# Kernel optimization log

Hardware: AMD Instinct MI355X
Metric: run time of the kernel (lower is better)

The kernel has to match this reference:

```python
import jax, jax.numpy as jnp
import numpy as np


def _rank_transform_ascending(flat):
    # torch: _, idx = sort(flat, descending=False); flat[idx] = linspace(0,1,n)+1/n
    n = flat.shape[0]
    order = jnp.argsort(flat)  # ascending
    prob = jnp.linspace(0.0, 1.0, n, dtype=flat.dtype) + jnp.asarray(1.0 / n, flat.dtype)
    return jnp.zeros_like(flat).at[order].set(prob)


def corr_attention(query, key, value):
    # score[b,h,i,j] = cosine-like similarity q_i . k_j / (|q_i| |k_j|)
    score = jnp.einsum('bhid,bhjd->bhij', query, key)
    q_len = jnp.sqrt(jnp.sum(query * query, axis=-1, keepdims=True)) + 1e-5  # [b,h,s,1]
    k_len = jnp.sqrt(jnp.sum(key * key, axis=-1, keepdims=True)) + 1e-5      # [b,h,s,1]
    score = score / (q_len * jnp.swapaxes(k_len, -1, -2))
    signal = jnp.sign(score)
    size = score.shape
    flat = jnp.abs(score).reshape(-1)
    ranked = _rank_transform_ascending(flat)
    score = -jnp.log(ranked).reshape(size) * signal
    score = score / jnp.sum(jnp.abs(score), axis=-1, keepdims=True)
    return jnp.einsum('bhij,bhjd->bhid', score, value)


def setup_inputs() -> dict:
    key0 = jax.random.key(0)
    kq, kk, kv = jax.random.split(key0, 3)
    B, H, S, D = 4, 8, 1024, 64
    query = jax.random.normal(kq, (B, H, S, D), dtype=jnp.float32)
    key = jax.random.normal(kk, (B, H, S, D), dtype=jnp.float32)
    value = jax.random.normal(kv, (B, H, S, D), dtype=jnp.float32)
    return {"query": query, "key": key, "value": value}


def reference(query, key, value):
    # Attention.forward with mode='season'
    return corr_attention(query, key, value)
```

## Files before the change

### kernel.cpp

```cpp
#include <hip/hip_runtime.h>
#include <math.h>
#include <stdint.h>

#define S_LEN 1024
#define D_DIM 64
#define BH    32
#define KSHIFT 13
#define NBINS 130048u
#define CODE_BASE 97280u
#define NB2   32768u
#define HIST_LO_C 20480u
#define NHOT_H  12288u
#define PV_LO_C 22528u
#define NPVT   10240u
#define NCHUNK 64
#define HBLK   256
#define INV_NM1 (1.0f/33554431.0f)
#define INV_N   (2.9802322387695312e-08f)
#define FIX_TH  1e-4f


typedef _Float16 half8 __attribute__((ext_vector_type(8)));
typedef short    short8 __attribute__((ext_vector_type(8)));
typedef float    floatx4 __attribute__((ext_vector_type(4)));

__device__ __forceinline__ void bf16_split(float x, short& hi, short& lo) {
  unsigned u = __float_as_uint(x);
  unsigned h = (u + 0x7FFFu + ((u >> 16) & 1u)) >> 16;
  float hf = __uint_as_float(h << 16);
  float lf = x - hf;
  hi = (short)h;
  lo = (short)(__float_as_uint(lf) >> 16);
}

__global__ __launch_bounds__(256) void norms_kernel(
    const float* __restrict__ Q, const float* __restrict__ K,
    double* __restrict__ qinvD, double* __restrict__ kinvD,
    unsigned short* __restrict__ Qhi_g, unsigned short* __restrict__ Qlo_g,
    unsigned short* __restrict__ Khi_g, unsigned short* __restrict__ Klo_g) {
  int row  = blockIdx.x * 4 + (threadIdx.x >> 6);
  int lane = threadIdx.x & 63;
  const float* src; double* dstD; unsigned short *hD, *lD; int r = row;
  if (row < BH * S_LEN) { src = Q; dstD = qinvD; hD = Qhi_g; lD = Qlo_g; }
  else { src = K; dstD = kinvD; hD = Khi_g; lD = Klo_g; r = row - BH * S_LEN; }
  float xf = src[(size_t)r * D_DIM + lane];
  double v = (double)xf;
  double s = v * v;
  #pragma unroll
  for (int off = 32; off; off >>= 1) s += __shfl_down(s, off);
  double inv = 0.0;
  if (lane == 0) {
    inv = 1.0 / (sqrt(s) + 1e-5);
    dstD[r] = inv;
  }
  inv = __shfl(inv, 0);
  float x = xf * (float)inv;
  short hi, lo;
  bf16_split(x, hi, lo);
  hD[(size_t)r * D_DIM + lane] = (unsigned short)hi;
  lD[(size_t)r * D_DIM + lane] = (unsigned short)lo;
}

__global__ __launch_bounds__(256) void qk_mfma_kernel(
    const float* __restrict__ Q, const float* __restrict__ K,
    const unsigned short* __restrict__ Qhi_g, const unsigned short* __restrict__ Qlo_g,
    const unsigned short* __restrict__ Khi_g, const unsigned short* __restrict__ Klo_g,
    const double* __restrict__ qinvD, const double* __restrict__ kinvD,
    unsigned short* __restrict__ code16) {
  __shared__ short Qhi[64][72], Qlo[64][72];
  __shared__ short Khi[64][72], Klo[64][72];
  int bh = blockIdx.z;
  int i0 = blockIdx.y * 64;
  int j0 = blockIdx.x * 64;
  int tid = threadIdx.x;
  {
    const unsigned short* Qh = Qhi_g + ((size_t)bh * S_LEN + i0) * D_DIM;
    const unsigned short* Ql = Qlo_g + ((size_t)bh * S_LEN + i0) * D_DIM;
    const unsigned short* Kh = Khi_g + ((size_t)bh * S_LEN + j0) * D_DIM;
    const unsigned short* Kl = Klo_g + ((size_t)bh * S_LEN + j0) * D_DIM;
    #pragma unroll
    for (int l = 0; l < 2; ++l) {
      int idx = l * 256 + tid;
      int row = idx >> 3, c = (idx & 7) * 8;
      *(uint4*)&Qhi[row][c] = *(const uint4*)(Qh + (size_t)row * D_DIM + c);
      *(uint4*)&Qlo[row][c] = *(const uint4*)(Ql + (size_t)row * D_DIM + c);
      *(uint4*)&Khi[row][c] = *(const uint4*)(Kh + (size_t)row * D_DIM + c);
      *(uint4*)&Klo[row][c] = *(const uint4*)(Kl + (size_t)row * D_DIM + c);
    }
  }
  __syncthreads();
  int wave = tid >> 6;
  int lane = tid & 63;
  int m    = lane & 15;
  int quad = lane >> 4;
  floatx4 acc[4];
  #pragma unroll
  for (int n = 0; n < 4; ++n) acc[n] = (floatx4){0.f, 0.f, 0.f, 0.f};
  #pragma unroll
  for (int ks = 0; ks < 2; ++ks) {
    int kb = ks * 32 + quad * 8;
    short8 a_hi = *(const short8*)&Qhi[wave * 16 + m][kb];
    short8 a_lo = *(const short8*)&Qlo[wave * 16 + m][kb];
    #pragma unroll
    for (int nt = 0; nt < 4; ++nt) {
      short8 b_hi = *(const short8*)&Khi[nt * 16 + m][kb];
      short8 b_lo = *(const short8*)&Klo[nt * 16 + m][kb];
      acc[nt] = __builtin_amdgcn_mfma_f32_16x16x32_bf16(a_hi, b_hi, acc[nt], 0, 0, 0);
      acc[nt] = __builtin_amdgcn_mfma_f32_16x16x32_bf16(a_hi, b_lo, acc[nt], 0, 0, 0);
      acc[nt] = __builtin_amdgcn_mfma_f32_16x16x32_bf16(a_lo, b_hi, acc[nt], 0, 0, 0);
    }
  }
  #pragma unroll
  for (int nt = 0; nt < 4; ++nt) {
    #pragma unroll
    for (int r = 0; r < 4; ++r) {
      unsigned long long am = __ballot(fabsf(acc[nt][r]) < FIX_TH);
      while (am) {
        int src = (int)(__ffsll((long long)am) - 1);
        am &= am - 1;
        int i_s = i0 + wave * 16 + (src >> 4) * 4 + r;
        int j_s = j0 + nt * 16 + (src & 15);
        double qd = (double)Q[((size_t)bh * S_LEN + i_s) * D_DIM + lane];
        double kd = (double)K[((size_t)bh * S_LEN + j_s) * D_DIM + lane];
        double pd = qd * kd;
        #pragma unroll
        for (int off = 32; off; off >>= 1) pd += __shfl_down(pd, off);
        float corr = 0.f;
        if (lane == 0)
          corr = (float)(pd * qinvD[(size_t)bh * S_LEN + i_s] * kinvD[(size_t)bh * S_LEN + j_s]);
        corr = __shfl(corr, 0);
        if (lane == src) acc[nt][r] = corr;
      }
    }
  }
  #pragma unroll
  for (int r = 0; r < 4; ++r) {
    unsigned short* op = code16 + (size_t)bh * 1048576 + (size_t)(j0 >> 6) * 65536
                       + (size_t)(i0 + wave * 16 + quad * 4 + r) * 64 + m;
    #pragma unroll
    for (int nt = 0; nt < 4; ++nt) {
      unsigned u = __float_as_uint(acc[nt][r]);
      unsigned a = u & 0x7fffffffu;
      unsigned b = a >> KSHIFT;
      if (b > NBINS - 1u) b = NBINS - 1u;
      unsigned c = (b < CODE_BASE) ? 0u : (b - CODE_BASE);
      op[nt * 16] = (unsigned short)(c | ((u >> 16) & 0x8000u));
    }
  }
}

__global__ __launch_bounds__(1024) void hist_kernel(
    const uint4* __restrict__ codes, unsigned* __restrict__ hist,
    unsigned char* __restrict__ partial) {
  __shared__ unsigned lh[NHOT_H];
  int tid = threadIdx.x;
  for (unsigned i = tid; i < NHOT_H; i += 1024) lh[i] = 0u;
  __syncthreads();
  const uint4* p = codes + (size_t)blockIdx.x * 16384;
  #pragma unroll 2
  for (int it = 0; it < 16; ++it) {
    uint4 w = p[it * 1024 + tid];
    unsigned ws[4] = {w.x, w.y, w.z, w.w};
    #pragma unroll
    for (int k = 0; k < 4; ++k) {
      unsigned c0 = ws[k] & 0x7fffu;
      unsigned c1 = (ws[k] >> 16) & 0x7fffu;
      if (c0 >= HIST_LO_C) atomicAdd(&lh[c0 - HIST_LO_C], 1u);
      else                 atomicAdd(&hist[c0], 1u);
      if (c1 >= HIST_LO_C) atomicAdd(&lh[c1 - HIST_LO_C], 1u);
      else                 atomicAdd(&hist[c1], 1u);
    }
  }
  __syncthreads();
  unsigned char* dst = partial + (size_t)blockIdx.x * NHOT_H;
  for (unsigned i = tid; i < NHOT_H; i += 1024) dst[i] = (unsigned char)lh[i];
}

__global__ __launch_bounds__(256) void hreduce_kernel(
    const unsigned char* __restrict__ partial, unsigned* __restrict__ hist) {
  unsigned bin = blockIdx.x * 256 + threadIdx.x;
  unsigned s = 0;
  #pragma unroll 8
  for (int b = 0; b < HBLK; ++b) s += (unsigned)partial[(size_t)b * NHOT_H + bin];
  hist[HIST_LO_C + bin] = s;
}

__global__ __launch_bounds__(256) void vt_kernel(
    const float* __restrict__ V, _Float16* __restrict__ Vt) {
  __shared__ _Float16 T[64][72];
  int bh = blockIdx.y, j0 = blockIdx.x * 64, tid = threadIdx.x;
  const float* Vb = V + ((size_t)bh * S_LEN + j0) * D_DIM;
  #pragma unroll
  for (int l = 0; l < 4; ++l) {
    int idx = l * 256 + tid;
    int jr = idx >> 4, d4 = idx & 15;
    float4 v = ((const float4*)Vb)[idx];
    T[d4*4+0][jr] = (_Float16)v.x;
    T[d4*4+1][jr] = (_Float16)v.y;
    T[d4*4+2][jr] = (_Float16)v.z;
    T[d4*4+3][jr] = (_Float16)v.w;
  }
  __syncthreads();
  _Float16* Ob = Vt + (size_t)(bh * 16 + blockIdx.x) * 4096;
  #pragma unroll
  for (int l = 0; l < 2; ++l) {
    int idx = l * 256 + tid;
    int d = idx >> 3, jc = idx & 7;
    uint4 val = *(const uint4*)&T[d][jc*8];
    *(uint4*)(Ob + (size_t)d * 64 + jc*8) = val;
  }
}

__global__ __launch_bounds__(256) void scan1_kernel(const unsigned* __restrict__ hist,
                                                    unsigned* __restrict__ csum) {
  __shared__ unsigned sd[256];
  int c = blockIdx.x, t = threadIdx.x;
  const unsigned* p = hist + (size_t)c * 512;
  sd[t] = p[t] + p[t + 256];
  __syncthreads();
  for (int off = 128; off; off >>= 1) {
    if (t < off) sd[t] += sd[t + off];
    __syncthreads();
  }
  if (t == 0) csum[c] = sd[0];
}

__global__ __launch_bounds__(256) void scan2_kernel(unsigned* __restrict__ csum) {
  __shared__ unsigned d[256];
  int t = threadIdx.x;
  unsigned v = (t < NCHUNK) ? csum[t] : 0u;
  d[t] = v; __syncthreads();
  for (int off = 1; off < 256; off <<= 1) {
    unsigned x = (t >= off) ? d[t - off] : 0u;
    __syncthreads();
    d[t] += x;
    __syncthreads();
  }
  if (t < NCHUNK) csum[t] = d[t] - v;
}

__global__ __launch_bounds__(256) void scan3_kernel(const unsigned* __restrict__ hist,
                                                    const unsigned* __restrict__ csum,
                                                    _Float16* __restrict__ tab2) {
  __shared__ unsigned ts[256];
  int c = blockIdx.x, t = threadIdx.x;
  const unsigned* p = hist + (size_t)c * 512 + t * 2;
  unsigned l0 = p[0], l1 = p[1];
  unsigned s = l0 + l1;
  ts[t] = s; __syncthreads();
  for (int off = 1; off < 256; off <<= 1) {
    unsigned x = (t >= off) ? ts[t - off] : 0u;
    __syncthreads();
    ts[t] += x;
    __syncthreads();
  }
  unsigned base = csum[c] + ts[t] - s;
  int idx = c * 512 + t * 2;
  float r0 = (float)base + 0.5f * ((float)l0 - 1.0f);
  tab2[idx]     = (_Float16)(-__logf(fmaf(r0, INV_NM1, INV_N)));
  float r1 = (float)(base + l0) + 0.5f * ((float)l1 - 1.0f);
  tab2[idx + 1] = (_Float16)(-__logf(fmaf(r1, INV_NM1, INV_N)));
}

__global__ __launch_bounds__(256) void pv_mfma_kernel(
    const unsigned short* __restrict__ code16, const _Float16* __restrict__ Vt,
    const unsigned short* __restrict__ tab2, float* __restrict__ out) {
  __shared__ unsigned short ldsT[NPVT];
  __shared__ float red[4352];
  int tid = threadIdx.x;

  int bh   = blockIdx.y;
  int wave = tid >> 6;
  int lane = tid & 63;
  int m    = lane & 15;
  int quad = lane >> 4;
  int i0   = blockIdx.x * 16;
  const unsigned short* Sb = code16 + (size_t)bh * 1048576 + (size_t)(i0 + m) * 64;
  const _Float16*       Vb = Vt + (size_t)bh * 65536;

  uint4 cw[8];
  #pragma unroll
  for (int ks = 0; ks < 8; ++ks) {
    int k0  = wave * 256 + ks * 32 + quad * 8;
    int jt  = k0 >> 6;
    int jin = k0 & 63;
    cw[ks] = *(const uint4*)(Sb + (size_t)jt * 65536 + jin);
  }

  {
    const unsigned* gsrc = (const unsigned*)(tab2 + PV_LO_C);
    unsigned* ldst = (unsigned*)ldsT;
    #pragma unroll
    for (int i = 0; i < 20; ++i)
      ldst[i * 256 + tid] = gsrc[i * 256 + tid];
  }
  __syncthreads();

  floatx4 acc[4];
  #pragma unroll
  for (int n = 0; n < 4; ++n) acc[n] = (floatx4){0.f, 0.f, 0.f, 0.f};
  float rsum = 0.f;

  #pragma unroll
  for (int ks = 0; ks < 8; ++ks) {
    int k0  = wave * 256 + ks * 32 + quad * 8;
    int jt  = k0 >> 6;
    int jin = k0 & 63;
    unsigned ww[4] = {cw[ks].x, cw[ks].y, cw[ks].z, cw[ks].w};
    union { unsigned short u[8]; half8 h; } af;
    #pragma unroll
    for (int e = 0; e < 8; ++e) {
      unsigned cd = (e & 1) ? (ww[e >> 1] >> 16) : (ww[e >> 1] & 0xffffu);
      unsigned c  = cd & 0x7fffu;
      unsigned sg = cd & 0x8000u;
      unsigned short tb;
      if (c >= PV_LO_C) tb = ldsT[c - PV_LO_C];
      else              tb = tab2[c];
      af.u[e] = (unsigned short)(tb ^ sg);
      unsigned short tabs = (unsigned short)(tb & 0x7fffu);
      _Float16 th = __builtin_bit_cast(_Float16, tabs);
      rsum += (float)th;
    }
    half8 bf[4];
    #pragma unroll
    for (int n = 0; n < 4; ++n)
      bf[n] = *(const half8*)(Vb + (size_t)jt * 4096 + (size_t)(n * 16 + m) * 64 + jin);
    #pragma unroll
    for (int n = 0; n < 4; ++n)
      acc[n] = __builtin_amdgcn_mfma_f32_16x16x32_f16(af.h, bf[n], acc[n], 0, 0, 0);
  }

  #pragma unroll
  for (int n = 0; n < 4; ++n)
    #pragma unroll
    for (int r = 0; r < 4; ++r)
      red[(wave * 16 + quad * 4 + r) * 64 + n * 16 + m] = acc[n][r];
  red[4096 + wave * 64 + lane] = rsum;
  __syncthreads();

  int col = tid & 63;
  int rq  = tid >> 6;
  #pragma unroll
  for (int t = 0; t < 4; ++t) {
    int row = rq * 4 + t;
    float s = 0.f;
    #pragma unroll
    for (int w = 0; w < 4; ++w) s += red[(w * 16 + row) * 64 + col];
    float rs = 0.f;
    #pragma unroll
    for (int w = 0; w < 4; ++w)
      #pragma unroll
      for (int q = 0; q < 4; ++q)
        rs += red[4096 + w * 64 + q * 16 + row];
    out[((size_t)bh * S_LEN + i0 + row) * D_DIM + col] = s / rs;
  }
}

extern "C" void kernel_launch(void* const* d_in, const int* in_sizes, int n_in,
                              void* d_out, int out_size, void* d_ws, size_t ws_size,
                              hipStream_t stream) {
  const float* Q = (const float*)d_in[0];
  const float* K = (const float*)d_in[1];
  const float* V = (const float*)d_in[2];
  float* out = (float*)d_out;
  char* ws = (char*)d_ws;
  unsigned short* code16  = (unsigned short*)(ws);
  unsigned*       hist    = (unsigned*)(ws + 67108864);
  unsigned char*  partial = (unsigned char*)(ws + 67239936);
  double*         qinvD   = (double*)(ws + 67239936 + 3145728);
  double*         kinvD   = (double*)(ws + 67239936 + 3407872);
  _Float16*       Vt      = (_Float16*)(ws + 67239936);
  unsigned*       csum    = (unsigned*)(ws + 67239936 + 4194304);
  _Float16*       tab2    = (_Float16*)(ws + 67239936 + 4195328);
  unsigned short* Qhi_g   = (unsigned short*)(ws + 71503872);
  unsigned short* Qlo_g   = (unsigned short*)(ws + 75698176);
  unsigned short* Khi_g   = (unsigned short*)(ws + 79892480);
  unsigned short* Klo_g   = (unsigned short*)(ws + 84086784);

  hipMemsetAsync(hist, 0, NB2 * sizeof(unsigned), stream);
  norms_kernel<<<(2 * BH * S_LEN) / 4, 256, 0, stream>>>(
      Q, K, qinvD, kinvD, Qhi_g, Qlo_g, Khi_g, Klo_g);
  qk_mfma_kernel<<<dim3(16, 16, BH), 256, 0, stream>>>(
      Q, K, Qhi_g, Qlo_g, Khi_g, Klo_g, qinvD, kinvD, code16);
  hist_kernel<<<HBLK, 1024, 0, stream>>>((const uint4*)code16, hist, partial);
  hreduce_kernel<<<NHOT_H / 256, 256, 0, stream>>>(partial, hist);
  vt_kernel<<<dim3(16, BH), 256, 0, stream>>>(V, Vt);
  scan1_kernel<<<NCHUNK, 256, 0, stream>>>(hist, csum);
  scan2_kernel<<<1, 256, 0, stream>>>(csum);
  scan3_kernel<<<NCHUNK, 256, 0, stream>>>(hist, csum, tab2);
  pv_mfma_kernel<<<dim3(S_LEN / 16, BH), 256, 0, stream>>>(
      code16, Vt, (const unsigned short*)tab2, out);
}
```

Before: 198.3 us.

## Stage code tiles in LDS and prefetch all V fragments before compute

The PV kernel now loads its 16-row code tile with fully coalesced 16-byte loads and stages it in shared memory. The table slice is loaded with vectorized uint4 loads. All V fragments for the eight k-steps are issued up front, so global latency overlaps before the MFMA loop. This raises register pressure (32 half8 values held live) and LDS usage by 32 KB, and launch bounds now request 2 blocks per CU, which may limit occupancy or cause spills.

```diff
diff --git a/kernel.cpp b/kernel.cpp
--- a/kernel.cpp
+++ b/kernel.cpp
@@ -262,10 +262,11 @@
   tab2[idx + 1] = (_Float16)(-__logf(fmaf(r1, INV_NM1, INV_N)));
 }
 
-__global__ __launch_bounds__(256) void pv_mfma_kernel(
+__global__ __launch_bounds__(256, 2) void pv_mfma_kernel(
     const unsigned short* __restrict__ code16, const _Float16* __restrict__ Vt,
     const unsigned short* __restrict__ tab2, float* __restrict__ out) {
   __shared__ unsigned short ldsT[NPVT];
+  __shared__ unsigned short codeT[16384];
   __shared__ float red[4352];
   int tid = threadIdx.x;
 
@@ -275,25 +276,38 @@
   int m    = lane & 15;
   int quad = lane >> 4;
   int i0   = blockIdx.x * 16;
-  const unsigned short* Sb = code16 + (size_t)bh * 1048576 + (size_t)(i0 + m) * 64;
+  const unsigned short* Cb = code16 + (size_t)bh * 1048576;
   const _Float16*       Vb = Vt + (size_t)bh * 65536;
 
-  uint4 cw[8];
+  uint4 ctmp[8];
+  #pragma unroll
+  for (int p = 0; p < 8; ++p) {
+    int c = p * 256 + tid;
+    int jt = c >> 7, row = (c >> 3) & 15, cin = c & 7;
+    ctmp[p] = *(const uint4*)(Cb + (size_t)jt * 65536 + (size_t)(i0 + row) * 64 + cin * 8);
+  }
+  uint4 ttmp[5];
+  #pragma unroll
+  for (int p = 0; p < 5; ++p)
+    ttmp[p] = *(const uint4*)(tab2 + PV_LO_C + (size_t)(p * 256 + tid) * 8);
+
+  half8 bf[8][4];
   #pragma unroll
   for (int ks = 0; ks < 8; ++ks) {
     int k0  = wave * 256 + ks * 32 + quad * 8;
     int jt  = k0 >> 6;
     int jin = k0 & 63;
-    cw[ks] = *(const uint4*)(Sb + (size_t)jt * 65536 + jin);
-  }
-
-  {
-    const unsigned* gsrc = (const unsigned*)(tab2 + PV_LO_C);
-    unsigned* ldst = (unsigned*)ldsT;
-    #pragma unroll
-    for (int i = 0; i < 20; ++i)
-      ldst[i * 256 + tid] = gsrc[i * 256 + tid];
-  }
+    #pragma unroll
+    for (int n = 0; n < 4; ++n)
+      bf[ks][n] = *(const half8*)(Vb + (size_t)jt * 4096 + (size_t)(n * 16 + m) * 64 + jin);
+  }
+
+  #pragma unroll
+  for (int p = 0; p < 8; ++p)
+    *(uint4*)&codeT[(p * 256 + tid) * 8] = ctmp[p];
+  #pragma unroll
+  for (int p = 0; p < 5; ++p)
+    *(uint4*)&ldsT[(p * 256 + tid) * 8] = ttmp[p];
   __syncthreads();
 
   floatx4 acc[4];
@@ -306,7 +320,8 @@
     int k0  = wave * 256 + ks * 32 + quad * 8;
     int jt  = k0 >> 6;
     int jin = k0 & 63;
-    unsigned ww[4] = {cw[ks].x, cw[ks].y, cw[ks].z, cw[ks].w};
+    uint4 w = *(const uint4*)&codeT[jt * 1024 + m * 64 + jin];
+    unsigned ww[4] = {w.x, w.y, w.z, w.w};
     union { unsigned short u[8]; half8 h; } af;
     #pragma unroll
     for (int e = 0; e < 8; ++e) {
@@ -321,13 +336,9 @@
       _Float16 th = __builtin_bit_cast(_Float16, tabs);
       rsum += (float)th;
     }
-    half8 bf[4];
     #pragma unroll
     for (int n = 0; n < 4; ++n)
-      bf[n] = *(const half8*)(Vb + (size_t)jt * 4096 + (size_t)(n * 16 + m) * 64 + jin);
-    #pragma unroll
-    for (int n = 0; n < 4; ++n)
-      acc[n] = __builtin_amdgcn_mfma_f32_16x16x32_f16(af.h, bf[n], acc[n], 0, 0, 0);
+      acc[n] = __builtin_amdgcn_mfma_f32_16x16x32_f16(af.h, bf[ks][n], acc[n], 0, 0, 0);
   }
 
   #pragma unroll
```

Result: no change. 202.1 us (+1.9%).

## Restructure PV kernel: full table in LDS, per-wave rows, no cross-wave reduction

Applied to the files above, without the earlier changes.

The PV kernel now loads the entire 32K-entry log-rank table into shared memory, so every lookup hits LDS instead of sometimes going to global. Each wave owns 16 query rows and walks the full key dimension, which removes the LDS cross-wave reduction and its barrier. Row sums are combined with shuffles, and code words are software-prefetched two steps ahead. The grid shrinks from 64 to 16 blocks per head, giving 512 blocks each holding 64 KB of LDS. That trades parallelism and occupancy for less redundant table loading and no reduction.

```diff
diff --git a/kernel.cpp b/kernel.cpp
--- a/kernel.cpp
+++ b/kernel.cpp
@@ -11,8 +11,6 @@
 #define NB2   32768u
 #define HIST_LO_C 20480u
 #define NHOT_H  12288u
-#define PV_LO_C 22528u
-#define NPVT   10240u
 #define NCHUNK 64
 #define HBLK   256
 #define INV_NM1 (1.0f/33554431.0f)
@@ -265,61 +263,58 @@
 __global__ __launch_bounds__(256) void pv_mfma_kernel(
     const unsigned short* __restrict__ code16, const _Float16* __restrict__ Vt,
     const unsigned short* __restrict__ tab2, float* __restrict__ out) {
-  __shared__ unsigned short ldsT[NPVT];
-  __shared__ float red[4352];
+  __shared__ unsigned short ldsT[NB2];
   int tid = threadIdx.x;
+  {
+    const uint4* gsrc = (const uint4*)tab2;
+    uint4* ldst = (uint4*)ldsT;
+    #pragma unroll
+    for (int i = 0; i < 16; ++i)
+      ldst[i * 256 + tid] = gsrc[i * 256 + tid];
+  }
+  __syncthreads();
 
   int bh   = blockIdx.y;
   int wave = tid >> 6;
   int lane = tid & 63;
   int m    = lane & 15;
   int quad = lane >> 4;
-  int i0   = blockIdx.x * 16;
+  int i0   = blockIdx.x * 64 + wave * 16;
   const unsigned short* Sb = code16 + (size_t)bh * 1048576 + (size_t)(i0 + m) * 64;
   const _Float16*       Vb = Vt + (size_t)bh * 65536;
 
-  uint4 cw[8];
-  #pragma unroll
-  for (int ks = 0; ks < 8; ++ks) {
-    int k0  = wave * 256 + ks * 32 + quad * 8;
+  floatx4 acc[4];
+  #pragma unroll
+  for (int n = 0; n < 4; ++n) acc[n] = (floatx4){0.f, 0.f, 0.f, 0.f};
+  float rsum = 0.f;
+
+  uint4 cwA, cwB;
+  {
+    int ka = 0 * 32 + quad * 8;
+    cwA = *(const uint4*)(Sb + (size_t)(ka >> 6) * 65536 + (ka & 63));
+    int kb = 1 * 32 + quad * 8;
+    cwB = *(const uint4*)(Sb + (size_t)(kb >> 6) * 65536 + (kb & 63));
+  }
+  #pragma unroll
+  for (int ks = 0; ks < 32; ++ks) {
+    uint4 cur = (ks & 1) ? cwB : cwA;
+    if (ks + 2 < 32) {
+      int kp = (ks + 2) * 32 + quad * 8;
+      uint4 nx = *(const uint4*)(Sb + (size_t)(kp >> 6) * 65536 + (kp & 63));
+      if (ks & 1) cwB = nx; else cwA = nx;
+    }
+    int k0  = ks * 32 + quad * 8;
     int jt  = k0 >> 6;
     int jin = k0 & 63;
-    cw[ks] = *(const uint4*)(Sb + (size_t)jt * 65536 + jin);
-  }
-
-  {
-    const unsigned* gsrc = (const unsigned*)(tab2 + PV_LO_C);
-    unsigned* ldst = (unsigned*)ldsT;
-    #pragma unroll
-    for (int i = 0; i < 20; ++i)
-      ldst[i * 256 + tid] = gsrc[i * 256 + tid];
-  }
-  __syncthreads();
-
-  floatx4 acc[4];
-  #pragma unroll
-  for (int n = 0; n < 4; ++n) acc[n] = (floatx4){0.f, 0.f, 0.f, 0.f};
-  float rsum = 0.f;
-
-  #pragma unroll
-  for (int ks = 0; ks < 8; ++ks) {
-    int k0  = wave * 256 + ks * 32 + quad * 8;
-    int jt  = k0 >> 6;
-    int jin = k0 & 63;
-    unsigned ww[4] = {cw[ks].x, cw[ks].y, cw[ks].z, cw[ks].w};
+    unsigned ww[4] = {cur.x, cur.y, cur.z, cur.w};
     union { unsigned short u[8]; half8 h; } af;
     #pragma unroll
     for (int e = 0; e < 8; ++e) {
       unsigned cd = (e & 1) ? (ww[e >> 1] >> 16) : (ww[e >> 1] & 0xffffu);
-      unsigned c  = cd & 0x7fffu;
-      unsigned sg = cd & 0x8000u;
-      unsigned short tb;
-      if (c >= PV_LO_C) tb = ldsT[c - PV_LO_C];
-      else              tb = tab2[c];
-      af.u[e] = (unsigned short)(tb ^ sg);
+      unsigned short tb = ldsT[cd & 0x7fffu];
+      af.u[e] = (unsigned short)(tb ^ (cd & 0x8000u));
       unsigned short tabs = (unsigned short)(tb & 0x7fffu);
-      _Float16 th = __builtin_bit_cast(_Float16, tabs);
-      rsum += (float)th;
+      rsum += (float)__builtin_bit_cast(_Float16, tabs);
     }
     half8 bf[4];
     #pragma unroll
@@ -330,29 +325,17 @@
       acc[n] = __builtin_amdgcn_mfma_f32_16x16x32_f16(af.h, bf[n], acc[n], 0, 0, 0);
   }
 
-  #pragma unroll
-  for (int n = 0; n < 4; ++n)
-    #pragma unroll
-    for (int r = 0; r < 4; ++r)
-      red[(wave * 16 + quad * 4 + r) * 64 + n * 16 + m] = acc[n][r];
-  red[4096 + wave * 64 + lane] = rsum;
-  __syncthreads();
-
-  int col = tid & 63;
-  int rq  = tid >> 6;
-  #pragma unroll
-  for (int t = 0; t < 4; ++t) {
-    int row = rq * 4 + t;
-    float s = 0.f;
-    #pragma unroll
-    for (int w = 0; w < 4; ++w) s += red[(w * 16 + row) * 64 + col];
-    float rs = 0.f;
-    #pragma unroll
-    for (int w = 0; w < 4; ++w)
-      #pragma unroll
-      for (int q = 0; q < 4; ++q)
-        rs += red[4096 + w * 64 + q * 16 + row];
-    out[((size_t)bh * S_LEN + i0 + row) * D_DIM + col] = s / rs;
+  rsum += __shfl_xor(rsum, 16);
+  rsum += __shfl_xor(rsum, 32);
+  float inv = 1.0f / rsum;
+  #pragma unroll
+  for (int r = 0; r < 4; ++r) {
+    int row = quad * 4 + r;
+    float invr = __shfl(inv, row);
+    float* op = out + ((size_t)bh * S_LEN + i0 + row) * D_DIM + m;
+    #pragma unroll
+    for (int n = 0; n < 4; ++n)
+      op[n * 16] = acc[n][r] * invr;
   }
 }
 
@@ -388,6 +371,6 @@
   scan1_kernel<<<NCHUNK, 256, 0, stream>>>(hist, csum);
   scan2_kernel<<<1, 256, 0, stream>>>(csum);
   scan3_kernel<<<NCHUNK, 256, 0, stream>>>(hist, csum, tab2);
-  pv_mfma_kernel<<<dim3(S_LEN / 16, BH), 256, 0, stream>>>(
+  pv_mfma_kernel<<<dim3(16, BH), 256, 0, stream>>>(
       code16, Vt, (const unsigned short*)tab2, out);
 }
```

After: 203.3 us. +2.5%, slower.
